# Kernel tuning notes

Measured on AMD Instinct MI355X. Metric: run time of the kernel, lower is better.

Reference implementation:

```python
import jax, jax.numpy as jnp
import numpy as np
import math
from math import factorial

L = 3            # SH degree -> (L+1)^2 = 16 basis functions
H = 1024         # coefficient grid height
W = 1024         # coefficient grid width
B = 1048576      # number of rays (1024x1024 render)


def _norm_lm(l, m):
    return math.sqrt((2 * l + 1) / (4 * math.pi) * (factorial(l - m) / factorial(l + m)))


def real_spherical_harmonics(dirs, L):
    """dirs: [N,3] float32 -> [N,(L+1)^2] float32 real SH basis."""
    eps = 1e-14
    r = jnp.linalg.norm(dirs, axis=-1) + eps
    xd, yd, zd = dirs[:, 0], dirs[:, 1], dirs[:, 2]
    theta = jnp.arccos(jnp.clip(zd / r, -1.0, 1.0))
    phi = jnp.arctan2(yd, xd)
    ct = jnp.cos(theta)
    # Associated Legendre P_l^m(ct) via the standard recursion (loops over the
    # small fixed (l,m) set unroll at trace time; all ops vectorized over N).
    p = {(0, 0): jnp.ones_like(ct)}
    if L >= 1:
        p[(1, 0)] = ct
        s = jnp.sqrt(jnp.clip(1.0 - ct * ct, 1e-14, None))
        p[(1, 1)] = s
        for l in range(2, L + 1):
            p[(l, l)] = (2 * l - 1) * s * p[(l - 1, l - 1)]
            for m in range(l - 1, -1, -1):
                a = (2 * l - 1) * ct * p[(l - 1, m)]
                b = (l + m - 1) * p[(l - 2, m)] if (l - 2) >= m else 0.0
                p[(l, m)] = (a - b) / (l - m)
    cols = []
    sqrt2 = math.sqrt(2.0)
    for l in range(L + 1):
        for m in range(-l, l + 1):
            if m == 0:
                cols.append(_norm_lm(l, 0) * p[(l, 0)])
            elif m > 0:
                sign = (-1.0) ** m
                cols.append(sqrt2 * sign * _norm_lm(l, m) * p[(l, m)] * jnp.cos(m * phi))
            else:
                mp = -m
                sign = (-1.0) ** m
                cols.append(sqrt2 * sign * _norm_lm(l, mp) * p[(l, mp)] * jnp.sin(mp * phi))
    return jnp.stack(cols, axis=-1)  # [N, (L+1)^2]


def setup_inputs() -> dict:
    key = jax.random.key(0)
    k1, k2, k3, k4 = jax.random.split(key, 4)
    return {
        "y": jax.random.randint(k1, (B,), 0, H),
        "x": jax.random.randint(k2, (B,), 0, W),
        "ray_dir": jax.random.normal(k3, (B, 3), dtype=jnp.float32),
        "sh_data": 0.1 * jax.random.normal(k4, (H, W, (L + 1) ** 2, 3), dtype=jnp.float32),
    }


def reference(y, x, ray_dir, sh_data):
    coefs = sh_data[y, x]                       # [B, (L+1)^2, 3] gather
    B_mat = real_spherical_harmonics(ray_dir, L)  # [B, (L+1)^2]
    c = jnp.einsum('bi,bij->bj', B_mat, coefs)    # [B, 3]
    return jnp.clip(c, 0.0, 1.0)
```

## Files before the change

kernel.cpp:

```cpp
#include <hip/hip_runtime.h>


#define SH_C0   0.28209479177387814f
#define SH_C1   0.48860251190291992f
#define SH_C2a  1.09254843059207907f
#define SH_C2b  0.31539156525252005f
#define SH_C2c  0.54627421529603959f
#define SH_C3a  0.59004358992664352f
#define SH_C3b  2.89061144264055405f
#define SH_C3c  0.45704579946446572f
#define SH_C3d  0.37317633259011546f
#define SH_C3e  1.44530572132027702f

__global__ __launch_bounds__(256) void sh_embed_kernel(
    const int* __restrict__ ys, const int* __restrict__ xs,
    const float* __restrict__ dirs, const float* __restrict__ sh,
    float* __restrict__ out, int B)
{
    int i = blockIdx.x * 256 + threadIdx.x;
    if (i >= B) return;

    int yy = ys[i];
    int xx = xs[i];
    const float4* __restrict__ c4 =
        (const float4*)(sh + (size_t)(yy * 1024 + xx) * 48u);

    float dx = dirs[3 * i + 0];
    float dy = dirs[3 * i + 1];
    float dz = dirs[3 * i + 2];
    float inv = rsqrtf(fmaf(dx, dx, fmaf(dy, dy, dz * dz)));
    float nx = dx * inv, ny = dy * inv, nz = dz * inv;

    float x2 = nx * nx, y2 = ny * ny, z2 = nz * nz;
    float xy = nx * ny, yz = ny * nz, xz = nx * nz;

    float b[16];
    b[0]  =  SH_C0;
    b[1]  = -SH_C1 * ny;
    b[2]  =  SH_C1 * nz;
    b[3]  = -SH_C1 * nx;
    b[4]  =  SH_C2a * xy;
    b[5]  = -SH_C2a * yz;
    b[6]  =  SH_C2b * (3.0f * z2 - 1.0f);
    b[7]  = -SH_C2a * xz;
    b[8]  =  SH_C2c * (x2 - y2);
    b[9]  = -SH_C3a * ny * (3.0f * x2 - y2);
    b[10] =  SH_C3b * xy * nz;
    b[11] = -SH_C3c * ny * (5.0f * z2 - 1.0f);
    b[12] =  SH_C3d * nz * (5.0f * z2 - 3.0f);
    b[13] = -SH_C3c * nx * (5.0f * z2 - 1.0f);
    b[14] =  SH_C3e * nz * (x2 - y2);
    b[15] = -SH_C3a * nx * (x2 - 3.0f * y2);

    float s0 = 0.0f, s1 = 0.0f, s2 = 0.0f;
#pragma unroll
    for (int j = 0; j < 12; ++j) {
        float4 v = c4[j];
        int k = 4 * j;
        {
            int k0 = k + 0;
            float* acc = (k0 % 3 == 0) ? &s0 : (k0 % 3 == 1) ? &s1 : &s2;
            *acc = fmaf(b[k0 / 3], v.x, *acc);
        }
        {
            int k1 = k + 1;
            float* acc = (k1 % 3 == 0) ? &s0 : (k1 % 3 == 1) ? &s1 : &s2;
            *acc = fmaf(b[k1 / 3], v.y, *acc);
        }
        {
            int k2 = k + 2;
            float* acc = (k2 % 3 == 0) ? &s0 : (k2 % 3 == 1) ? &s1 : &s2;
            *acc = fmaf(b[k2 / 3], v.z, *acc);
        }
        {
            int k3 = k + 3;
            float* acc = (k3 % 3 == 0) ? &s0 : (k3 % 3 == 1) ? &s1 : &s2;
            *acc = fmaf(b[k3 / 3], v.w, *acc);
        }
    }

    out[3 * i + 0] = fminf(fmaxf(s0, 0.0f), 1.0f);
    out[3 * i + 1] = fminf(fmaxf(s1, 0.0f), 1.0f);
    out[3 * i + 2] = fminf(fmaxf(s2, 0.0f), 1.0f);
}

extern "C" void kernel_launch(void* const* d_in, const int* in_sizes, int n_in,
                              void* d_out, int out_size, void* d_ws, size_t ws_size,
                              hipStream_t stream) {
    const int*   ys   = (const int*)d_in[0];
    const int*   xs   = (const int*)d_in[1];
    const float* dirs = (const float*)d_in[2];
    const float* sh   = (const float*)d_in[3];
    float* out = (float*)d_out;
    int B = in_sizes[0];
    int blocks = (B + 255) / 256;
    sh_embed_kernel<<<blocks, 256, 0, stream>>>(ys, xs, dirs, sh, out, B);
}
```

Measured before the change: 296.0 us.

## Split each ray's coefficient gather across four cooperating lanes with shuffle reduction

Each ray is now handled by four adjacent threads. Each thread loads three float4s of the 192-byte coefficient record, interleaved so the four lanes together read contiguous 64-byte chunks. Each thread applies its share of FMAs using a per-lane switch, and the partial sums are combined with xor shuffles before three lanes write the outputs. This targets the scattered, uncoalesced per-thread 192-byte gathers and adds parallelism for hiding latency. The cost is that the SH basis math and direction loads are repeated four times, plus extra shuffles and divergence from the switch.

```diff
diff --git a/kernel.cpp b/kernel.cpp
--- a/kernel.cpp
+++ b/kernel.cpp
@@ -12,27 +12,39 @@
 #define SH_C3d  0.37317633259011546f
 #define SH_C3e  1.44530572132027702f
 
-__global__ __launch_bounds__(256) void sh_embed_kernel(
+#define DO4(v, J0,C0, J1,C1, J2,C2, J3,C3)        \
+    s##C0 = fmaf(b[J0], (v).x, s##C0);            \
+    s##C1 = fmaf(b[J1], (v).y, s##C1);            \
+    s##C2 = fmaf(b[J2], (v).z, s##C2);            \
+    s##C3 = fmaf(b[J3], (v).w, s##C3);
+
+__global__ __launch_bounds__(256) void sh_embed_coop(
     const int* __restrict__ ys, const int* __restrict__ xs,
     const float* __restrict__ dirs, const float* __restrict__ sh,
     float* __restrict__ out, int B)
 {
-    int i = blockIdx.x * 256 + threadIdx.x;
-    if (i >= B) return;
+    const int tid  = blockIdx.x * 256 + threadIdx.x;
+    const int ray  = tid >> 2;
+    const int q    = tid & 3;
+    if (ray >= B) return;
 
-    int yy = ys[i];
-    int xx = xs[i];
+    const int yy = ys[ray];
+    const int xx = xs[ray];
     const float4* __restrict__ c4 =
         (const float4*)(sh + (size_t)(yy * 1024 + xx) * 48u);
 
-    float dx = dirs[3 * i + 0];
-    float dy = dirs[3 * i + 1];
-    float dz = dirs[3 * i + 2];
-    float inv = rsqrtf(fmaf(dx, dx, fmaf(dy, dy, dz * dz)));
-    float nx = dx * inv, ny = dy * inv, nz = dz * inv;
+    const float4 v0 = c4[q];
+    const float4 v1 = c4[q + 4];
+    const float4 v2 = c4[q + 8];
 
-    float x2 = nx * nx, y2 = ny * ny, z2 = nz * nz;
-    float xy = nx * ny, yz = ny * nz, xz = nx * nz;
+    const float dx = dirs[3 * ray + 0];
+    const float dy = dirs[3 * ray + 1];
+    const float dz = dirs[3 * ray + 2];
+    const float inv = rsqrtf(fmaf(dx, dx, fmaf(dy, dy, dz * dz)));
+    const float nx = dx * inv, ny = dy * inv, nz = dz * inv;
+
+    const float x2 = nx * nx, y2 = ny * ny, z2 = nz * nz;
+    const float xy = nx * ny, yz = ny * nz, xz = nx * nz;
 
     float b[16];
     b[0]  =  SH_C0;
@@ -53,35 +65,37 @@
     b[15] = -SH_C3a * nx * (x2 - 3.0f * y2);
 
     float s0 = 0.0f, s1 = 0.0f, s2 = 0.0f;
-#pragma unroll
-    for (int j = 0; j < 12; ++j) {
-        float4 v = c4[j];
-        int k = 4 * j;
-        {
-            int k0 = k + 0;
-            float* acc = (k0 % 3 == 0) ? &s0 : (k0 % 3 == 1) ? &s1 : &s2;
-            *acc = fmaf(b[k0 / 3], v.x, *acc);
-        }
-        {
-            int k1 = k + 1;
-            float* acc = (k1 % 3 == 0) ? &s0 : (k1 % 3 == 1) ? &s1 : &s2;
-            *acc = fmaf(b[k1 / 3], v.y, *acc);
-        }
-        {
-            int k2 = k + 2;
-            float* acc = (k2 % 3 == 0) ? &s0 : (k2 % 3 == 1) ? &s1 : &s2;
-            *acc = fmaf(b[k2 / 3], v.z, *acc);
-        }
-        {
-            int k3 = k + 3;
-            float* acc = (k3 % 3 == 0) ? &s0 : (k3 % 3 == 1) ? &s1 : &s2;
-            *acc = fmaf(b[k3 / 3], v.w, *acc);
-        }
+    switch (q) {
+    case 0:
+        DO4(v0,  0,0,  0,1,  0,2,  1,0)
+        DO4(v1,  5,1,  5,2,  6,0,  6,1)
+        DO4(v2, 10,2, 11,0, 11,1, 11,2)
+        break;
+    case 1:
+        DO4(v0,  1,1,  1,2,  2,0,  2,1)
+        DO4(v1,  6,2,  7,0,  7,1,  7,2)
+        DO4(v2, 12,0, 12,1, 12,2, 13,0)
+        break;
+    case 2:
+        DO4(v0,  2,2,  3,0,  3,1,  3,2)
+        DO4(v1,  8,0,  8,1,  8,2,  9,0)
+        DO4(v2, 13,1, 13,2, 14,0, 14,1)
+        break;
+    default:
+        DO4(v0,  4,0,  4,1,  4,2,  5,0)
+        DO4(v1,  9,1,  9,2, 10,0, 10,1)
+        DO4(v2, 14,2, 15,0, 15,1, 15,2)
+        break;
     }
 
-    out[3 * i + 0] = fminf(fmaxf(s0, 0.0f), 1.0f);
-    out[3 * i + 1] = fminf(fmaxf(s1, 0.0f), 1.0f);
-    out[3 * i + 2] = fminf(fmaxf(s2, 0.0f), 1.0f);
+    s0 += __shfl_xor(s0, 1, 64);  s0 += __shfl_xor(s0, 2, 64);
+    s1 += __shfl_xor(s1, 1, 64);  s1 += __shfl_xor(s1, 2, 64);
+    s2 += __shfl_xor(s2, 1, 64);  s2 += __shfl_xor(s2, 2, 64);
+
+    if (q < 3) {
+        float val = (q == 0) ? s0 : (q == 1) ? s1 : s2;
+        out[(size_t)3 * ray + q] = fminf(fmaxf(val, 0.0f), 1.0f);
+    }
 }
 
 extern "C" void kernel_launch(void* const* d_in, const int* in_sizes, int n_in,
@@ -93,6 +107,6 @@
     const float* sh   = (const float*)d_in[3];
     float* out = (float*)d_out;
     int B = in_sizes[0];
-    int blocks = (B + 255) / 256;
-    sh_embed_kernel<<<blocks, 256, 0, stream>>>(ys, xs, dirs, sh, out, B);
+    int blocks = (B + 63) / 64;
+    sh_embed_coop<<<blocks, 256, 0, stream>>>(ys, xs, dirs, sh, out, B);
 }
```

Result: faster. 287.9 us (-2.7%).
